# Kernel tuning notes

Hardware: AMD Instinct MI355X
Metric: run time of the kernel (lower is better)

Reference implementation:

```python
import jax, jax.numpy as jnp
import numpy as np

B, T, D, H = 8, 4096, 1024, 1024


def log_g(x):
    # log of g(x) = relu(x)+0.5 for x>=0, sigmoid(x) for x<0 (continuous at 0)
    return jnp.where(x >= 0, jnp.log(jax.nn.relu(x) + 0.5), -jax.nn.softplus(-x))


def setup_inputs() -> dict:
    key = jax.random.key(0)
    k0, k1, k2, k3, k4, k5 = jax.random.split(key, 6)
    s = 1.0 / np.sqrt(D)
    return {
        "x": jax.random.normal(k0, (B, T, D), jnp.float32),
        "h_0": jax.random.normal(k1, (B, H), jnp.float32),
        "Wz": jax.random.uniform(k2, (H, D), jnp.float32, -s, s),
        "bz": jax.random.uniform(k3, (H,), jnp.float32, -s, s),
        "Wh": jax.random.uniform(k4, (H, D), jnp.float32, -s, s),
        "bh": jax.random.uniform(k5, (H,), jnp.float32, -s, s),
    }


def reference(x, h_0, Wz, bz, Wh, bh):
    # gate pre-activation k: (B,T,H)
    k = jnp.einsum("btd,hd->bth", x, Wz) + bz
    log_z = -jax.nn.softplus(-k)        # log sigmoid(k)
    log_coeffs = -jax.nn.softplus(k)    # log (1 - sigmoid(k))
    log_h_0 = log_g(h_0)[:, None, :]    # (B,1,H)
    log_tilde_h = log_g(jnp.einsum("btd,hd->bth", x, Wh) + bh)
    log_values = jnp.concatenate([log_h_0, log_z + log_tilde_h], axis=1)  # (B,T+1,H)
    # parallel scan in log space
    a_star = jnp.pad(jnp.cumsum(log_coeffs, axis=1), ((0, 0), (1, 0), (0, 0)))
    log_h = a_star + jax.lax.cumlogsumexp(log_values - a_star, axis=1)
    h = jnp.exp(log_h)                  # (B,T+1,H)
    return h[:, -T:, :]
```

## Files before the change

kernel.cpp:

```cpp
#include <hip/hip_runtime.h>
#include <hip/hip_bf16.h>

#define Bb 8
#define Tt 4096
#define Dd 1024
#define Hh 1024
#define Mm (Bb * Tt)
#define NCHUNK 32
#define CLEN 128

typedef float f32x4 __attribute__((ext_vector_type(4)));
typedef short bf16x8 __attribute__((ext_vector_type(8)));

__device__ __forceinline__ unsigned f2bfu(float x) {
  unsigned u = __float_as_uint(x);
  return (u + 0x7fffu + ((u >> 16) & 1u)) >> 16;
}
__device__ __forceinline__ float bflo(unsigned u) { return __uint_as_float(u << 16); }
__device__ __forceinline__ float bfhi(unsigned u) { return __uint_as_float(u & 0xffff0000u); }

__global__ void cvt_kernel(const float* __restrict__ src, unsigned short* __restrict__ dst,
                           int n4) {
  int i = blockIdx.x * blockDim.x + threadIdx.x;
  int stride = gridDim.x * blockDim.x;
  for (; i < n4; i += stride) {
    float4 v = reinterpret_cast<const float4*>(src)[i];
    ushort4 o;
    o.x = (unsigned short)f2bfu(v.x);
    o.y = (unsigned short)f2bfu(v.y);
    o.z = (unsigned short)f2bfu(v.z);
    o.w = (unsigned short)f2bfu(v.w);
    reinterpret_cast<ushort4*>(dst)[i] = o;
  }
}

__device__ __forceinline__ void async16(const unsigned short* g, unsigned short* l) {
  __builtin_amdgcn_global_load_lds(
      (const __attribute__((address_space(1))) unsigned int*)g,
      (__attribute__((address_space(3))) unsigned int*)l, 16, 0, 0);
}

__global__ void __launch_bounds__(512, 4) gemm_kernel(
    const unsigned short* __restrict__ xb,
    const unsigned short* __restrict__ wzb,
    const unsigned short* __restrict__ whb,
    const float* __restrict__ bz,
    const float* __restrict__ bh,
    unsigned int* __restrict__ P) {
  __shared__ unsigned short lds[36864];
  const int tid = threadIdx.x;
  const int wid = tid >> 6;
  const int wm = wid >> 2;
  const int wn = wid & 3;
  const int l = tid & 63, ln = l & 15, l4 = l >> 4;

  const int id = blockIdx.x;
  const int sw = (id & 7) * 256 + (id >> 3);
  const int mb = sw >> 3, nb = sw & 7;
  const int m0 = mb * 128, h0 = nb * 128;

  const int r0 = tid >> 2;
  const int chunk = ((tid & 3) - (r0 >> 1)) & 3;
  const unsigned short* agp = xb + (size_t)(m0 + r0) * Dd + chunk * 8;
  const int sub16 = r0 >> 4;
  const int hrow0 = h0 + ((sub16 >> 1) << 4) + (r0 & 15);
  const unsigned short* bgp =
      ((sub16 & 1) ? whb : wzb) + (size_t)hrow0 * Dd + chunk * 8;
  const int ta = tid * 8;

  auto stage = [&](int buf) {
    unsigned short* d = &lds[buf * 12288];
    async16(agp, d + ta);
    async16(bgp, d + 4096 + ta);
    async16(bgp + (size_t)64 * Dd, d + 8192 + ta);
    agp += 32;
    bgp += 32;
  };

  int oA[4], oB[4];
#pragma unroll
  for (int mf = 0; mf < 4; ++mf) {
    const int row = wm * 64 + mf * 16 + ln;
    const int sl = (l4 + (row >> 1)) & 3;
    oA[mf] = row * 32 + sl * 8;
  }
#pragma unroll
  for (int nf = 0; nf < 4; ++nf) {
    const int row = wn * 64 + nf * 16 + ln;
    const int sl = (l4 + (row >> 1)) & 3;
    oB[nf] = 4096 + row * 32 + sl * 8;
  }

  f32x4 acc[4][4];
#pragma unroll
  for (int i = 0; i < 4; ++i)
#pragma unroll
    for (int j = 0; j < 4; ++j) acc[i][j] = f32x4{0.f, 0.f, 0.f, 0.f};

  stage(0);
  stage(1);

  int cur = 0, nxt = 2;
#pragma unroll 1
  for (int s = 0; s < 32; ++s) {
    asm volatile("s_waitcnt vmcnt(3)" ::: "memory");
    __builtin_amdgcn_s_barrier();
    const unsigned short* bp = &lds[cur * 12288];
    bf16x8 af[4], bf[4];
    af[0] = *(const bf16x8*)(bp + oA[0]);
    af[1] = *(const bf16x8*)(bp + oA[1]);
    af[2] = *(const bf16x8*)(bp + oA[2]);
    af[3] = *(const bf16x8*)(bp + oA[3]);
    bf[0] = *(const bf16x8*)(bp + oB[0]);
    bf[1] = *(const bf16x8*)(bp + oB[1]);
    bf[2] = *(const bf16x8*)(bp + oB[2]);
    bf[3] = *(const bf16x8*)(bp + oB[3]);
    stage(nxt);
    __builtin_amdgcn_s_setprio(1);
#pragma unroll
    for (int i = 0; i < 4; ++i)
#pragma unroll
      for (int j = 0; j < 4; ++j)
        acc[i][j] =
            __builtin_amdgcn_mfma_f32_16x16x32_bf16(af[i], bf[j], acc[i][j], 0, 0, 0);
    __builtin_amdgcn_s_setprio(0);
    cur = (cur + 1) == 3 ? 0 : cur + 1;
    nxt = (nxt + 1) == 3 ? 0 : nxt + 1;
  }

  asm volatile("s_waitcnt vmcnt(0)" ::: "memory");

#pragma unroll
  for (int p = 0; p < 2; ++p) {
    const int hcol = h0 + (wn * 2 + p) * 16 + ln;
    const float bzv = bz[hcol];
    const float bhv = bh[hcol];
#pragma unroll
    for (int mf = 0; mf < 4; ++mf) {
#pragma unroll
      for (int q = 0; q < 4; ++q) {
        const int m = m0 + wm * 64 + mf * 16 + l4 * 4 + q;
        const float kv = acc[mf][2 * p][q] + bzv;
        const float pv = acc[mf][2 * p + 1][q] + bhv;
        const float ek = __expf(kv);
        const float a = 1.f / (1.f + ek);
        const float z = 1.f - a;
        const float g = (pv >= 0.f) ? (pv + 0.5f) : (1.f / (1.f + __expf(-pv)));
        const float c = z * g;
        P[(size_t)m * Hh + hcol] = f2bfu(a) | (f2bfu(c) << 16);
      }
    }
  }
}

__global__ void scan_pass1(const unsigned int* __restrict__ P,
                           float* __restrict__ Pp, float* __restrict__ Qq) {
  const int h = blockIdx.x * 256 + threadIdx.x;
  const int ch = blockIdx.y;
  const int b = blockIdx.z;
  const unsigned int* p = P + ((size_t)(b * Tt + ch * CLEN)) * Hh + h;
  float A = 1.f, Q = 0.f;
#pragma unroll 8
  for (int i = 0; i < CLEN; ++i) {
    const unsigned u = p[(size_t)i * Hh];
    Q = fmaf(bflo(u), Q, bfhi(u));
    A *= bflo(u);
  }
  const int idx = ch * (Bb * Hh) + b * Hh + h;
  Pp[idx] = A;
  Qq[idx] = Q;
}

__global__ void scan_pass2(const float* __restrict__ h0raw,
                           const float* __restrict__ Pp, const float* __restrict__ Qq,
                           float* __restrict__ Hinit) {
  const int bh = blockIdx.x * 256 + threadIdx.x;
  const float x = h0raw[bh];
  float hs = (x >= 0.f) ? (x + 0.5f) : (1.f / (1.f + __expf(-x)));
  for (int ch = 0; ch < NCHUNK; ++ch) {
    const int idx = ch * (Bb * Hh) + bh;
    Hinit[idx] = hs;
    hs = fmaf(Pp[idx], hs, Qq[idx]);
  }
}

__global__ void scan_pass3(const unsigned int* __restrict__ P,
                           const float* __restrict__ Hinit,
                           float* __restrict__ out) {
  const int h = blockIdx.x * 256 + threadIdx.x;
  const int ch = blockIdx.y;
  const int b = blockIdx.z;
  float hs = Hinit[ch * (Bb * Hh) + b * Hh + h];
  const size_t base = ((size_t)(b * Tt + ch * CLEN)) * Hh + h;
  const unsigned int* p = P + base;
  float* o = out + base;
#pragma unroll 8
  for (int i = 0; i < CLEN; ++i) {
    const unsigned u = p[(size_t)i * Hh];
    hs = fmaf(bflo(u), hs, bfhi(u));
    o[(size_t)i * Hh] = hs;
  }
}

extern "C" void kernel_launch(void* const* d_in, const int* in_sizes, int n_in,
                              void* d_out, int out_size, void* d_ws, size_t ws_size,
                              hipStream_t stream) {
  const float* x  = (const float*)d_in[0];
  const float* h0 = (const float*)d_in[1];
  const float* Wz = (const float*)d_in[2];
  const float* bz = (const float*)d_in[3];
  const float* Wh = (const float*)d_in[4];
  const float* bh = (const float*)d_in[5];
  float* out = (float*)d_out;

  char* ws = (char*)d_ws;
  unsigned short* xb  = (unsigned short*)(ws);
  unsigned short* wzb = (unsigned short*)(ws + 67108864);
  unsigned short* whb = (unsigned short*)(ws + 69206016);
  unsigned int*   P   = (unsigned int*)(ws + 71303168);
  float* Pp    = (float*)(ws + 205520896);
  float* Qq    = (float*)(ws + 206569472);
  float* Hinit = (float*)(ws + 207618048);

  cvt_kernel<<<4096, 256, 0, stream>>>(x, xb, Mm * Dd / 4);
  cvt_kernel<<<1024, 256, 0, stream>>>(Wz, wzb, Hh * Dd / 4);
  cvt_kernel<<<1024, 256, 0, stream>>>(Wh, whb, Hh * Dd / 4);

  gemm_kernel<<<2048, 512, 0, stream>>>(xb, wzb, whb, bz, bh, P);

  dim3 sgrid(Hh / 256, NCHUNK, Bb);
  scan_pass1<<<sgrid, 256, 0, stream>>>(P, Pp, Qq);
  scan_pass2<<<Bb * Hh / 256, 256, 0, stream>>>(h0, Pp, Qq, Hinit);
  scan_pass3<<<sgrid, 256, 0, stream>>>(P, Hinit, out);
}
```

Measured before the change: 277.7 us.

## Fuse chunk-summary scan pass into GEMM epilogue via warp shuffles

Removes the separate scan_pass1 kernel. Each GEMM block now computes the per-chunk (A, Q) affine-composition summary for its 128 rows directly from the bf16-rounded gate values, using a per-thread serial compose, xor-shuffle compose across lane groups, and an LDS reduction across the two warp rows. This avoids re-reading the 128 MB P buffer once and saves a kernel launch, at the cost of extra epilogue work and an added block barrier in the GEMM. The LDS swizzle for A/B tiles is also changed from (row>>1) to row-based rotation.

Result: faster. 266.0 us (-4.2%).

```diff
diff --git a/kernel.cpp b/kernel.cpp
--- a/kernel.cpp
+++ b/kernel.cpp
@@ -40,13 +40,26 @@
       (__attribute__((address_space(3))) unsigned int*)l, 16, 0, 0);
 }
 
+#define SHFL_COMPOSE(A, Q, MASK, HIBIT)                                   \
+  {                                                                       \
+    const float pA_ = __shfl_xor(A, MASK);                                \
+    const float pQ_ = __shfl_xor(Q, MASK);                                \
+    const float Alo_ = (HIBIT) ? pA_ : A;                                 \
+    const float Qlo_ = (HIBIT) ? pQ_ : Q;                                 \
+    const float Ahi_ = (HIBIT) ? A : pA_;                                 \
+    const float Qhi_ = (HIBIT) ? Q : pQ_;                                 \
+    A = Alo_ * Ahi_;                                                      \
+    Q = fmaf(Ahi_, Qlo_, Qhi_);                                           \
+  }
+
 __global__ void __launch_bounds__(512, 4) gemm_kernel(
     const unsigned short* __restrict__ xb,
     const unsigned short* __restrict__ wzb,
     const unsigned short* __restrict__ whb,
     const float* __restrict__ bz,
     const float* __restrict__ bh,
-    unsigned int* __restrict__ P) {
+    unsigned int* __restrict__ P,
+    float* __restrict__ Pp, float* __restrict__ Qq) {
   __shared__ unsigned short lds[36864];
   const int tid = threadIdx.x;
   const int wid = tid >> 6;
@@ -60,7 +73,7 @@
   const int m0 = mb * 128, h0 = nb * 128;
 
   const int r0 = tid >> 2;
-  const int chunk = ((tid & 3) - (r0 >> 1)) & 3;
+  const int chunk = ((tid & 3) - r0) & 3;
   const unsigned short* agp = xb + (size_t)(m0 + r0) * Dd + chunk * 8;
   const int sub16 = r0 >> 4;
   const int hrow0 = h0 + ((sub16 >> 1) << 4) + (r0 & 15);
@@ -81,13 +94,13 @@
 #pragma unroll
   for (int mf = 0; mf < 4; ++mf) {
     const int row = wm * 64 + mf * 16 + ln;
-    const int sl = (l4 + (row >> 1)) & 3;
+    const int sl = (l4 + row) & 3;
     oA[mf] = row * 32 + sl * 8;
   }
 #pragma unroll
   for (int nf = 0; nf < 4; ++nf) {
     const int row = wn * 64 + nf * 16 + ln;
-    const int sl = (l4 + (row >> 1)) & 3;
+    const int sl = (l4 + row) & 3;
     oB[nf] = 4096 + row * 32 + sl * 8;
   }
 
@@ -129,14 +142,22 @@
   }
 
   asm volatile("s_waitcnt vmcnt(0)" ::: "memory");
+  __syncthreads();
+
+  float* sA = (float*)lds;
+  float* sQ = (float*)lds + 256;
+  const int b_idx = mb >> 5;
+  const int ch = mb & 31;
 
 #pragma unroll
   for (int p = 0; p < 2; ++p) {
     const int hcol = h0 + (wn * 2 + p) * 16 + ln;
     const float bzv = bz[hcol];
     const float bhv = bh[hcol];
+    float Ar = 1.f, Qr = 0.f;
 #pragma unroll
     for (int mf = 0; mf < 4; ++mf) {
+      float A4 = 1.f, Q4 = 0.f;
 #pragma unroll
       for (int q = 0; q < 4; ++q) {
         const int m = m0 + wm * 64 + mf * 16 + l4 * 4 + q;
@@ -147,28 +168,30 @@
         const float z = 1.f - a;
         const float g = (pv >= 0.f) ? (pv + 0.5f) : (1.f / (1.f + __expf(-pv)));
         const float c = z * g;
-        P[(size_t)m * Hh + hcol] = f2bfu(a) | (f2bfu(c) << 16);
+        const unsigned pw = f2bfu(a) | (f2bfu(c) << 16);
+        P[(size_t)m * Hh + hcol] = pw;
+        const float ar = bflo(pw), cr = bfhi(pw);
+        Q4 = fmaf(ar, Q4, cr);
+        A4 *= ar;
       }
+      SHFL_COMPOSE(A4, Q4, 16, (l4 & 1));
+      SHFL_COMPOSE(A4, Q4, 32, ((l4 >> 1) & 1));
+      Qr = fmaf(A4, Qr, Q4);
+      Ar *= A4;
     }
-  }
-}
-
-__global__ void scan_pass1(const unsigned int* __restrict__ P,
-                           float* __restrict__ Pp, float* __restrict__ Qq) {
-  const int h = blockIdx.x * 256 + threadIdx.x;
-  const int ch = blockIdx.y;
-  const int b = blockIdx.z;
-  const unsigned int* p = P + ((size_t)(b * Tt + ch * CLEN)) * Hh + h;
-  float A = 1.f, Q = 0.f;
-#pragma unroll 8
-  for (int i = 0; i < CLEN; ++i) {
-    const unsigned u = p[(size_t)i * Hh];
-    Q = fmaf(bflo(u), Q, bfhi(u));
-    A *= bflo(u);
-  }
-  const int idx = ch * (Bb * Hh) + b * Hh + h;
-  Pp[idx] = A;
-  Qq[idx] = Q;
+    if (l4 == 0) {
+      sA[wm * 128 + (wn * 2 + p) * 16 + ln] = Ar;
+      sQ[wm * 128 + (wn * 2 + p) * 16 + ln] = Qr;
+    }
+  }
+  __syncthreads();
+  if (tid < 128) {
+    const float A0 = sA[tid], Q0 = sQ[tid];
+    const float A1 = sA[128 + tid], Q1 = sQ[128 + tid];
+    const int idx = ch * (Bb * Hh) + b_idx * Hh + (h0 + tid);
+    Pp[idx] = A0 * A1;
+    Qq[idx] = fmaf(A1, Q0, Q1);
+  }
 }
 
 __global__ void scan_pass2(const float* __restrict__ h0raw,
@@ -226,10 +249,9 @@
   cvt_kernel<<<1024, 256, 0, stream>>>(Wz, wzb, Hh * Dd / 4);
   cvt_kernel<<<1024, 256, 0, stream>>>(Wh, whb, Hh * Dd / 4);
 
-  gemm_kernel<<<2048, 512, 0, stream>>>(xb, wzb, whb, bz, bh, P);
-
+  gemm_kernel<<<2048, 512, 0, stream>>>(xb, wzb, whb, bz, bh, P, Pp, Qq);
+
+  scan_pass2<<<Bb * Hh / 256, 256, 0, stream>>>(h0, Pp, Qq, Hinit);
   dim3 sgrid(Hh / 256, NCHUNK, Bb);
-  scan_pass1<<<sgrid, 256, 0, stream>>>(P, Pp, Qq);
-  scan_pass2<<<Bb * Hh / 256, 256, 0, stream>>>(h0, Pp, Qq, Hinit);
   scan_pass3<<<sgrid, 256, 0, stream>>>(P, Hinit, out);
 }
```
